# Kernel tuning notes

Hardware: AMD Instinct MI355X
Metric: run time of the kernel (lower is better)

The kernel has to match this reference:

```python
import jax, jax.numpy as jnp
import numpy as np

EMBED = 768
HEAD = 128

def setup_inputs() -> dict:
    key = jax.random.key(0)
    ks = jax.random.split(key, 8)
    B, S = 8, 2048
    x = jax.random.normal(ks[0], (B, S, EMBED), dtype=jnp.float32)
    enc_output = jax.random.normal(ks[1], (B, S, EMBED), dtype=jnp.float32)
    s = 1.0 / np.sqrt(EMBED)
    Wq = jax.random.normal(ks[2], (EMBED, HEAD), dtype=jnp.float32) * s
    Wk = jax.random.normal(ks[3], (EMBED, HEAD), dtype=jnp.float32) * s
    Wv = jax.random.normal(ks[4], (EMBED, HEAD), dtype=jnp.float32) * s
    bq = jnp.zeros((HEAD,), dtype=jnp.float32)
    bk = jnp.zeros((HEAD,), dtype=jnp.float32)
    bv = jnp.zeros((HEAD,), dtype=jnp.float32)
    return {"x": x, "enc_output": enc_output, "Wq": Wq, "bq": bq,
            "Wk": Wk, "bk": bk, "Wv": Wv, "bv": bv}

def reference(x, enc_output, Wq, bq, Wk, bk, Wv, bv):
    # Faithful to original: Q, K, V all from x (enc_output is unused in the
    # original forward); scale is embed_size ** 0.5; dropout never applied.
    q = jnp.einsum('nse,ed->nsd', x, Wq) + bq  # [B,S,H]
    k = jnp.einsum('nse,ed->nsd', x, Wk) + bk
    v = jnp.einsum('nse,ed->nsd', x, Wv) + bv
    energy = jnp.einsum('nqd,nkd->nqk', q, k)  # [B,S,S]
    attn = jax.nn.softmax(energy / jnp.sqrt(jnp.float32(EMBED)), axis=2)
    out = jnp.einsum('nql,nld->nqd', attn, v)  # [B,S,H]
    return out
```

## Files before the change

### kernel.cpp

```cpp
#include <hip/hip_runtime.h>
#include <hip/hip_bf16.h>


typedef __bf16 bf16x8 __attribute__((ext_vector_type(8)));
typedef float f32x4 __attribute__((ext_vector_type(4)));
using bf16 = __hip_bfloat16;

#define EMB 768
#define HD 128
#define SEQ 2048
#define BATCH 8
#define ROWS (BATCH * SEQ)
#define NSPLIT 4
#define TILES_PER_SPLIT (SEQ / 64 / NSPLIT)

__global__ __launch_bounds__(256) void wt_kernel(
    const float* __restrict__ Wq, const float* __restrict__ Wk,
    const float* __restrict__ Wv, bf16* __restrict__ Wt)
{
    __shared__ float t_lds[32][33];
    const int tid = threadIdx.x;
    const int k0 = blockIdx.x * 32;
    const int n0 = blockIdx.y * 32;
    const int mtx = blockIdx.z;
    const float* W = (mtx == 0) ? Wq : (mtx == 1) ? Wk : Wv;
    const int j = tid & 31, i0 = tid >> 5;
#pragma unroll
    for (int c = 0; c < 4; ++c)
        t_lds[i0 + 8 * c][j] = W[(size_t)(k0 + i0 + 8 * c) * HD + n0 + j];
    __syncthreads();
#pragma unroll
    for (int c = 0; c < 4; ++c)
        Wt[(size_t)mtx * HD * EMB + (size_t)(n0 + i0 + 8 * c) * EMB + k0 + j] =
            __float2bfloat16(t_lds[j][i0 + 8 * c]);
}

__global__ __launch_bounds__(256, 3) void qkv_kernel(
    const float* __restrict__ x, const bf16* __restrict__ Wt,
    const float* __restrict__ bq, const float* __restrict__ bk,
    const float* __restrict__ bv,
    bf16* __restrict__ Q, bf16* __restrict__ K, bf16* __restrict__ Vt)
{
    __shared__ alignas(16) bf16 b_lds[2][128 * 64];
    const int tid  = threadIdx.x;
    const int sel  = blockIdx.y;
    const int row0 = blockIdx.x * 64;
    const int lane = tid & 63, wave = tid >> 6;
    const int lr = lane & 15, lq = lane >> 4;

    const char* Wb = (const char*)(Wt + (size_t)sel * HD * EMB);
    const int rl = lane >> 3;
    const int chlog = (lane & 7) ^ rl;

    const float* arow = &x[(size_t)(row0 + wave * 16 + lr) * EMB + lq * 8];

    float4 araw[2][2];
    auto loadA = [&](int kt) {
#pragma unroll
        for (int ks = 0; ks < 2; ++ks) {
            const float* p = arow + kt * 64 + ks * 32;
            araw[ks][0] = *reinterpret_cast<const float4*>(p);
            araw[ks][1] = *reinterpret_cast<const float4*>(p + 4);
        }
    };
    auto stageB = [&](int kt, int pb) {
#pragma unroll
        for (int c = 0; c < 4; ++c) {
            int r = c * 32 + wave * 8 + rl;
            const char* src = Wb + (size_t)r * (EMB * 2) + kt * 128 + chlog * 16;
            bf16* dst = &b_lds[pb][(size_t)(c * 32 + wave * 8) * 64];
            __builtin_amdgcn_global_load_lds(
                (const __attribute__((address_space(1))) void*)src,
                (__attribute__((address_space(3))) void*)dst, 16, 0, 0);
        }
    };

    f32x4 acc[8];
#pragma unroll
    for (int j = 0; j < 8; ++j) acc[j] = f32x4{0.f, 0.f, 0.f, 0.f};

    stageB(0, 0);
    loadA(0);
    __syncthreads();

    for (int kt = 0; kt < EMB / 64; ++kt) {
        const int p = kt & 1;
        if (kt < 11) stageB(kt + 1, p ^ 1);
        bf16x8 af[2];
#pragma unroll
        for (int ks = 0; ks < 2; ++ks) {
            union { bf16 h[8]; bf16x8 v; } u;
            u.h[0] = __float2bfloat16(araw[ks][0].x);
            u.h[1] = __float2bfloat16(araw[ks][0].y);
            u.h[2] = __float2bfloat16(araw[ks][0].z);
            u.h[3] = __float2bfloat16(araw[ks][0].w);
            u.h[4] = __float2bfloat16(araw[ks][1].x);
            u.h[5] = __float2bfloat16(araw[ks][1].y);
            u.h[6] = __float2bfloat16(araw[ks][1].z);
            u.h[7] = __float2bfloat16(araw[ks][1].w);
            af[ks] = u.v;
        }
        if (kt < 11) loadA(kt + 1);
#pragma unroll
        for (int ks = 0; ks < 2; ++ks)
#pragma unroll
            for (int nt = 0; nt < 8; ++nt) {
                const bf16x8 b = *reinterpret_cast<const bf16x8*>(
                    &b_lds[p][((nt * 16 + lr) * 8 + ((ks * 4 + lq) ^ (lr & 7))) * 8]);
                acc[nt] = __builtin_amdgcn_mfma_f32_16x16x32_bf16(af[ks], b, acc[nt], 0, 0, 0);
            }
        __syncthreads();
    }

    bf16 (*o_lds)[132] = reinterpret_cast<bf16(*)[132]>(&b_lds[0][0]);
    const float* bias = (sel == 0) ? bq : (sel == 1) ? bk : bv;
#pragma unroll
    for (int nt = 0; nt < 8; ++nt) {
        int col = nt * 16 + lr;
        float bb = bias[col];
#pragma unroll
        for (int rg = 0; rg < 4; ++rg)
            o_lds[wave * 16 + lq * 4 + rg][col] = __float2bfloat16(acc[nt][rg] + bb);
    }
    __syncthreads();
    if (sel < 2) {
        bf16* dst = (sel == 0) ? Q : K;
#pragma unroll
        for (int c = 0; c < 4; ++c) {
            int lin = tid + c * 256;
            int r = lin >> 4, ch = lin & 15;
            *reinterpret_cast<uint4*>(&dst[(size_t)(row0 + r) * HD + ch * 8]) =
                *reinterpret_cast<const uint4*>(&o_lds[r][ch * 8]);
        }
    } else {
        int d = tid >> 1, sh = (tid & 1) * 32;
        int bi = row0 >> 11, s0 = row0 & (SEQ - 1);
        union { bf16 h[32]; uint4 u4[4]; } pk;
#pragma unroll
        for (int s = 0; s < 32; ++s) pk.h[s] = o_lds[sh + s][d];
        bf16* base = &Vt[((size_t)bi * HD + d) * SEQ + s0 + sh];
#pragma unroll
        for (int c = 0; c < 4; ++c)
            *reinterpret_cast<uint4*>(base + c * 8) = pk.u4[c];
    }
}

__global__ __launch_bounds__(256, 2) void flash_kernel(
    const bf16* __restrict__ Q, const bf16* __restrict__ K,
    const bf16* __restrict__ Vt,
    float* __restrict__ Opart, float* __restrict__ Lpart)
{
    __shared__ alignas(16) bf16 k_lds[64][132];
    __shared__ alignas(16) bf16 v_lds[144][68];
    __shared__ alignas(16) bf16 p_lds[4][32][72];
    const int tid = threadIdx.x;
    const int lane = tid & 63, wave = tid >> 6;
    const int lr = lane & 15, lq = lane >> 4;
    const int b  = blockIdx.y;
    const int split = blockIdx.z;
    const int q0 = blockIdx.x * 128;
    const int qrow = b * SEQ + q0 + wave * 32;

    const float sc = 0.03608439182435161f * 1.44269504088896f;

    for (int i = tid; i < 16 * 68; i += 256) {
        int r = i / 68, c = i % 68;
        v_lds[128 + r][c] = __float2bfloat16(r == 0 ? 1.0f : 0.0f);
    }

    bf16x8 qf[2][4];
#pragma unroll
    for (int qt = 0; qt < 2; ++qt)
#pragma unroll
        for (int ks = 0; ks < 4; ++ks)
            qf[qt][ks] = *reinterpret_cast<const bf16x8*>(
                &Q[(size_t)(qrow + qt * 16 + lr) * HD + ks * 32 + lq * 8]);

    f32x4 o[2][9];
#pragma unroll
    for (int qt = 0; qt < 2; ++qt)
#pragma unroll
        for (int d = 0; d < 9; ++d) o[qt][d] = f32x4{0.f, 0.f, 0.f, 0.f};

    for (int t = split * TILES_PER_SPLIT; t < (split + 1) * TILES_PER_SPLIT; ++t) {
        __syncthreads();
#pragma unroll
        for (int c = 0; c < 4; ++c) {
            int lin = tid + c * 256;
            int r = lin >> 4, ch = lin & 15;
            *reinterpret_cast<uint4*>(&k_lds[r][ch * 8]) =
                *reinterpret_cast<const uint4*>(&K[(size_t)(b * SEQ + t * 64 + r) * HD + ch * 8]);
        }
#pragma unroll
        for (int c = 0; c < 4; ++c) {
            int lin = tid + c * 256;
            int r = lin >> 3, ch = lin & 7;
            *reinterpret_cast<uint4*>(&v_lds[r][ch * 8]) =
                *reinterpret_cast<const uint4*>(&Vt[((size_t)b * HD + r) * SEQ + t * 64 + ch * 8]);
        }
        __syncthreads();

#pragma unroll
        for (int nt = 0; nt < 4; ++nt) {
            bf16x8 kf[4];
#pragma unroll
            for (int ks = 0; ks < 4; ++ks)
                kf[ks] = *reinterpret_cast<const bf16x8*>(&k_lds[nt * 16 + lr][ks * 32 + lq * 8]);
#pragma unroll
            for (int qt = 0; qt < 2; ++qt) {
                f32x4 s = f32x4{0.f, 0.f, 0.f, 0.f};
#pragma unroll
                for (int ks = 0; ks < 4; ++ks)
                    s = __builtin_amdgcn_mfma_f32_16x16x32_bf16(kf[ks], qf[qt][ks], s, 0, 0, 0);
                union { bf16 h[4]; uint2 u; } pk;
#pragma unroll
                for (int r = 0; r < 4; ++r)
                    pk.h[r] = __float2bfloat16(exp2f(__builtin_fmaf(s[r], sc, -8.0f)));
                *reinterpret_cast<uint2*>(&p_lds[wave][qt * 16 + lr][nt * 16 + lq * 4]) = pk.u;
            }
        }

#pragma unroll
        for (int ks = 0; ks < 2; ++ks) {
            bf16x8 pf[2];
#pragma unroll
            for (int qt = 0; qt < 2; ++qt)
                pf[qt] = *reinterpret_cast<const bf16x8*>(
                    &p_lds[wave][qt * 16 + lr][ks * 32 + lq * 8]);
#pragma unroll
            for (int d = 0; d < 9; ++d) {
                bf16x8 vf = *reinterpret_cast<const bf16x8*>(&v_lds[d * 16 + lr][ks * 32 + lq * 8]);
#pragma unroll
                for (int qt = 0; qt < 2; ++qt)
                    o[qt][d] = __builtin_amdgcn_mfma_f32_16x16x32_bf16(vf, pf[qt], o[qt][d], 0, 0, 0);
            }
        }
    }

    const size_t obase = (size_t)split * ROWS;
#pragma unroll
    for (int qt = 0; qt < 2; ++qt) {
#pragma unroll
        for (int d = 0; d < 8; ++d)
            *reinterpret_cast<f32x4*>(
                &Opart[(obase + qrow + qt * 16 + lr) * HD + d * 16 + lq * 4]) = o[qt][d];
        if (lane < 16)
            Lpart[obase + qrow + qt * 16 + lr] = o[qt][8][0];
    }
}

__global__ __launch_bounds__(256) void combine_kernel(
    const float* __restrict__ Opart, const float* __restrict__ Lpart,
    float* __restrict__ out)
{
    int gid = blockIdx.x * 256 + threadIdx.x;
    int row = gid >> 5, dc = gid & 31;
    float L = 0.f;
#pragma unroll
    for (int s = 0; s < NSPLIT; ++s)
        L += Lpart[(size_t)s * ROWS + row];
    float4 acc = {0.f, 0.f, 0.f, 0.f};
#pragma unroll
    for (int s = 0; s < NSPLIT; ++s) {
        float4 v = *reinterpret_cast<const float4*>(&Opart[((size_t)s * ROWS + row) * HD + dc * 4]);
        acc.x += v.x; acc.y += v.y; acc.z += v.z; acc.w += v.w;
    }
    float inv = 1.f / L;
    acc.x *= inv; acc.y *= inv; acc.z *= inv; acc.w *= inv;
    *reinterpret_cast<float4*>(&out[(size_t)row * HD + dc * 4]) = acc;
}

extern "C" void kernel_launch(void* const* d_in, const int* in_sizes, int n_in,
                              void* d_out, int out_size, void* d_ws, size_t ws_size,
                              hipStream_t stream) {
    const float* x  = (const float*)d_in[0];
    const float* Wq = (const float*)d_in[2];
    const float* bq = (const float*)d_in[3];
    const float* Wk = (const float*)d_in[4];
    const float* bk = (const float*)d_in[5];
    const float* Wv = (const float*)d_in[6];
    const float* bv = (const float*)d_in[7];
    float* out = (float*)d_out;

    char* ws = (char*)d_ws;
    const size_t WT_BYTES  = (size_t)3 * HD * EMB * 2;
    const size_t QKV_BYTES = (size_t)ROWS * HD * 2;
    const size_t OP_BYTES  = (size_t)NSPLIT * ROWS * HD * 4;
    bf16*  Wt    = (bf16*)ws;
    bf16*  Qb    = (bf16*)(ws + WT_BYTES);
    bf16*  Kb    = (bf16*)(ws + WT_BYTES + QKV_BYTES);
    bf16*  Vt    = (bf16*)(ws + WT_BYTES + 2 * QKV_BYTES);
    float* Opart = (float*)(ws + WT_BYTES + 3 * QKV_BYTES);
    float* Lpart = (float*)(ws + WT_BYTES + 3 * QKV_BYTES + OP_BYTES);

    hipLaunchKernelGGL(wt_kernel, dim3(EMB / 32, HD / 32, 3), dim3(256), 0, stream,
                       Wq, Wk, Wv, Wt);
    hipLaunchKernelGGL(qkv_kernel, dim3(ROWS / 64, 3), dim3(256), 0, stream,
                       x, Wt, bq, bk, bv, Qb, Kb, Vt);
    hipLaunchKernelGGL(flash_kernel, dim3(SEQ / 128, BATCH, NSPLIT), dim3(256), 0, stream,
                       Qb, Kb, Vt, Opart, Lpart);
    hipLaunchKernelGGL(combine_kernel, dim3(ROWS * 32 / 256), dim3(256), 0, stream,
                       Opart, Lpart, out);
}
```

Measured before the change: 181.8 us.

## Fuse Q, K, V projections into one block per row tile

The QKV projection kernel now computes all three outputs in one 512-thread block: 8 waves split as 4 row groups by 2 column halves of the 384-wide concatenated weight. Each x row tile is read and converted to bf16 once instead of three times, and the grid drops its third dimension. The cost is doubled LDS per block for the B tiles (96KB double buffer), 12 accumulators per wave, and a reworked epilogue that writes Q, K and the transposed V from one staging buffer. Lower occupancy could limit the gain.

Measured after the change: 183.8 us. Within noise of the previous version (+1.1%).

```diff
diff --git a/kernel.cpp b/kernel.cpp
--- a/kernel.cpp
+++ b/kernel.cpp
@@ -35,24 +35,25 @@
             __float2bfloat16(t_lds[j][i0 + 8 * c]);
 }
 
-__global__ __launch_bounds__(256, 3) void qkv_kernel(
+__global__ __launch_bounds__(512, 2) void qkv_kernel(
     const float* __restrict__ x, const bf16* __restrict__ Wt,
     const float* __restrict__ bq, const float* __restrict__ bk,
     const float* __restrict__ bv,
     bf16* __restrict__ Q, bf16* __restrict__ K, bf16* __restrict__ Vt)
 {
-    __shared__ alignas(16) bf16 b_lds[2][128 * 64];
+    __shared__ alignas(16) bf16 b_lds[2][384 * 64];
     const int tid  = threadIdx.x;
-    const int sel  = blockIdx.y;
     const int row0 = blockIdx.x * 64;
     const int lane = tid & 63, wave = tid >> 6;
     const int lr = lane & 15, lq = lane >> 4;
-
-    const char* Wb = (const char*)(Wt + (size_t)sel * HD * EMB);
+    const int wr = wave >> 1;
+    const int cw = wave & 1;
+
+    const char* Wb = (const char*)Wt;
     const int rl = lane >> 3;
     const int chlog = (lane & 7) ^ rl;
 
-    const float* arow = &x[(size_t)(row0 + wave * 16 + lr) * EMB + lq * 8];
+    const float* arow = &x[(size_t)(row0 + wr * 16 + lr) * EMB + lq * 8];
 
     float4 araw[2][2];
     auto loadA = [&](int kt) {
@@ -65,19 +66,19 @@
     };
     auto stageB = [&](int kt, int pb) {
 #pragma unroll
-        for (int c = 0; c < 4; ++c) {
-            int r = c * 32 + wave * 8 + rl;
+        for (int c = 0; c < 6; ++c) {
+            int r = c * 64 + wave * 8 + rl;
             const char* src = Wb + (size_t)r * (EMB * 2) + kt * 128 + chlog * 16;
-            bf16* dst = &b_lds[pb][(size_t)(c * 32 + wave * 8) * 64];
+            bf16* dst = &b_lds[pb][(size_t)(c * 64 + wave * 8) * 64];
             __builtin_amdgcn_global_load_lds(
                 (const __attribute__((address_space(1))) void*)src,
                 (__attribute__((address_space(3))) void*)dst, 16, 0, 0);
         }
     };
 
-    f32x4 acc[8];
-#pragma unroll
-    for (int j = 0; j < 8; ++j) acc[j] = f32x4{0.f, 0.f, 0.f, 0.f};
+    f32x4 acc[12];
+#pragma unroll
+    for (int j = 0; j < 12; ++j) acc[j] = f32x4{0.f, 0.f, 0.f, 0.f};
 
     stageB(0, 0);
     loadA(0);
@@ -104,44 +105,47 @@
 #pragma unroll
         for (int ks = 0; ks < 2; ++ks)
 #pragma unroll
-            for (int nt = 0; nt < 8; ++nt) {
+            for (int nt = 0; nt < 12; ++nt) {
                 const bf16x8 b = *reinterpret_cast<const bf16x8*>(
-                    &b_lds[p][((nt * 16 + lr) * 8 + ((ks * 4 + lq) ^ (lr & 7))) * 8]);
+                    &b_lds[p][((cw * 192 + nt * 16 + lr) * 8 + ((ks * 4 + lq) ^ (lr & 7))) * 8]);
                 acc[nt] = __builtin_amdgcn_mfma_f32_16x16x32_bf16(af[ks], b, acc[nt], 0, 0, 0);
             }
         __syncthreads();
     }
 
-    bf16 (*o_lds)[132] = reinterpret_cast<bf16(*)[132]>(&b_lds[0][0]);
-    const float* bias = (sel == 0) ? bq : (sel == 1) ? bk : bv;
-#pragma unroll
-    for (int nt = 0; nt < 8; ++nt) {
-        int col = nt * 16 + lr;
-        float bb = bias[col];
-#pragma unroll
-        for (int rg = 0; rg < 4; ++rg)
-            o_lds[wave * 16 + lq * 4 + rg][col] = __float2bfloat16(acc[nt][rg] + bb);
+    bf16* o_lds = &b_lds[0][0];
+    {
+#pragma unroll
+        for (int nt = 0; nt < 12; ++nt) {
+            int colb = cw * 192 + nt * 16;
+            int m = colb >> 7;
+            const float* bp = (m == 0) ? bq : (m == 1) ? bk : bv;
+            float bb = bp[(colb & 127) + lr];
+#pragma unroll
+            for (int rg = 0; rg < 4; ++rg)
+                o_lds[(wr * 16 + lq * 4 + rg) * 400 + colb + lr] =
+                    __float2bfloat16(acc[nt][rg] + bb);
+        }
     }
     __syncthreads();
-    if (sel < 2) {
-        bf16* dst = (sel == 0) ? Q : K;
-#pragma unroll
-        for (int c = 0; c < 4; ++c) {
-            int lin = tid + c * 256;
-            int r = lin >> 4, ch = lin & 15;
-            *reinterpret_cast<uint4*>(&dst[(size_t)(row0 + r) * HD + ch * 8]) =
-                *reinterpret_cast<const uint4*>(&o_lds[r][ch * 8]);
-        }
-    } else {
-        int d = tid >> 1, sh = (tid & 1) * 32;
+#pragma unroll
+    for (int c = 0; c < 4; ++c) {
+        int lin = c * 512 + tid;
+        int r = lin >> 5, ch = lin & 31;
+        uint4 v = *reinterpret_cast<const uint4*>(&o_lds[r * 400 + ch * 8]);
+        bf16* dst = (ch < 16) ? &Q[(size_t)(row0 + r) * HD + ch * 8]
+                              : &K[(size_t)(row0 + r) * HD + (ch - 16) * 8];
+        *reinterpret_cast<uint4*>(dst) = v;
+    }
+    {
+        int d = tid >> 2, sh = (tid & 3) * 16;
         int bi = row0 >> 11, s0 = row0 & (SEQ - 1);
-        union { bf16 h[32]; uint4 u4[4]; } pk;
-#pragma unroll
-        for (int s = 0; s < 32; ++s) pk.h[s] = o_lds[sh + s][d];
+        union { bf16 h[16]; uint4 u4[2]; } pk;
+#pragma unroll
+        for (int i = 0; i < 16; ++i) pk.h[i] = o_lds[(sh + i) * 400 + 256 + d];
         bf16* base = &Vt[((size_t)bi * HD + d) * SEQ + s0 + sh];
-#pragma unroll
-        for (int c = 0; c < 4; ++c)
-            *reinterpret_cast<uint4*>(base + c * 8) = pk.u4[c];
+        *reinterpret_cast<uint4*>(base)     = pk.u4[0];
+        *reinterpret_cast<uint4*>(base + 8) = pk.u4[1];
     }
 }
 
@@ -295,7 +299,7 @@
 
     hipLaunchKernelGGL(wt_kernel, dim3(EMB / 32, HD / 32, 3), dim3(256), 0, stream,
                        Wq, Wk, Wv, Wt);
-    hipLaunchKernelGGL(qkv_kernel, dim3(ROWS / 64, 3), dim3(256), 0, stream,
+    hipLaunchKernelGGL(qkv_kernel, dim3(ROWS / 64), dim3(512), 0, stream,
                        x, Wt, bq, bk, bv, Qb, Kb, Vt);
     hipLaunchKernelGGL(flash_kernel, dim3(SEQ / 128, BATCH, NSPLIT), dim3(256), 0, stream,
                        Qb, Kb, Vt, Opart, Lpart);
```

## Double-buffer K/V tiles with direct global-to-LDS loads and 512-thread blocks

Applied to the files above, without the earlier changes.

The flash kernel now stages K and V tiles into two LDS buffers with the direct global-to-LDS load builtin, prefetching the next tile while the current one is computed, and drops one of the two barriers per iteration. LDS rows use an XOR swizzle instead of padding to avoid bank conflicts. Blocks grow to 512 threads covering 256 query rows, so each K/V tile is shared by twice as many waves. The cost is higher LDS use per block, which may limit occupancy, and reliance on the async-load ordering being correct without an explicit wait.

Measured after the change: 182.6 us. About the same (+0.4%).

```diff
diff --git a/kernel.cpp b/kernel.cpp
--- a/kernel.cpp
+++ b/kernel.cpp
@@ -145,28 +145,56 @@
     }
 }
 
-__global__ __launch_bounds__(256, 2) void flash_kernel(
+__global__ __launch_bounds__(512, 2) void flash_kernel(
     const bf16* __restrict__ Q, const bf16* __restrict__ K,
     const bf16* __restrict__ Vt,
     float* __restrict__ Opart, float* __restrict__ Lpart)
 {
-    __shared__ alignas(16) bf16 k_lds[64][132];
-    __shared__ alignas(16) bf16 v_lds[144][68];
-    __shared__ alignas(16) bf16 p_lds[4][32][72];
+    __shared__ alignas(16) bf16 k_lds[2][64][128];
+    __shared__ alignas(16) bf16 v_lds[2][144][64];
+    __shared__ alignas(16) bf16 p_lds[8][32][72];
     const int tid = threadIdx.x;
     const int lane = tid & 63, wave = tid >> 6;
     const int lr = lane & 15, lq = lane >> 4;
     const int b  = blockIdx.y;
     const int split = blockIdx.z;
-    const int q0 = blockIdx.x * 128;
+    const int q0 = blockIdx.x * 256;
     const int qrow = b * SEQ + q0 + wave * 32;
 
     const float sc = 0.03608439182435161f * 1.44269504088896f;
 
-    for (int i = tid; i < 16 * 68; i += 256) {
-        int r = i / 68, c = i % 68;
-        v_lds[128 + r][c] = __float2bfloat16(r == 0 ? 1.0f : 0.0f);
-    }
+    for (int i = tid; i < 2 * 16 * 64; i += 512) {
+        int pb = i >> 10, r = (i >> 6) & 15, c = i & 63;
+        v_lds[pb][128 + r][c] = __float2bfloat16(r == 0 ? 1.0f : 0.0f);
+    }
+
+    const int rl16 = lane >> 4, sl16 = lane & 15;
+    const int rl8  = lane >> 3, sl8  = lane & 7;
+
+    auto stage = [&](int t, int pb) {
+#pragma unroll
+        for (int c = 0; c < 2; ++c) {
+            int rbase = c * 32 + wave * 4;
+            int r = rbase + rl16;
+            int ch = sl16 ^ (r & 7);
+            const bf16* src = &K[(size_t)(b * SEQ + t * 64 + r) * HD + ch * 8];
+            bf16* dst = &k_lds[pb][rbase][0];
+            __builtin_amdgcn_global_load_lds(
+                (const __attribute__((address_space(1))) void*)src,
+                (__attribute__((address_space(3))) void*)dst, 16, 0, 0);
+        }
+#pragma unroll
+        for (int c = 0; c < 2; ++c) {
+            int rbase = c * 64 + wave * 8;
+            int r = rbase + rl8;
+            int ch = sl8 ^ (r & 7);
+            const bf16* src = &Vt[((size_t)b * HD + r) * SEQ + t * 64 + ch * 8];
+            bf16* dst = &v_lds[pb][rbase][0];
+            __builtin_amdgcn_global_load_lds(
+                (const __attribute__((address_space(1))) void*)src,
+                (__attribute__((address_space(3))) void*)dst, 16, 0, 0);
+        }
+    };
 
     bf16x8 qf[2][4];
 #pragma unroll
@@ -182,30 +210,21 @@
 #pragma unroll
         for (int d = 0; d < 9; ++d) o[qt][d] = f32x4{0.f, 0.f, 0.f, 0.f};
 
-    for (int t = split * TILES_PER_SPLIT; t < (split + 1) * TILES_PER_SPLIT; ++t) {
-        __syncthreads();
-#pragma unroll
-        for (int c = 0; c < 4; ++c) {
-            int lin = tid + c * 256;
-            int r = lin >> 4, ch = lin & 15;
-            *reinterpret_cast<uint4*>(&k_lds[r][ch * 8]) =
-                *reinterpret_cast<const uint4*>(&K[(size_t)(b * SEQ + t * 64 + r) * HD + ch * 8]);
-        }
-#pragma unroll
-        for (int c = 0; c < 4; ++c) {
-            int lin = tid + c * 256;
-            int r = lin >> 3, ch = lin & 7;
-            *reinterpret_cast<uint4*>(&v_lds[r][ch * 8]) =
-                *reinterpret_cast<const uint4*>(&Vt[((size_t)b * HD + r) * SEQ + t * 64 + ch * 8]);
-        }
-        __syncthreads();
+    const int t0 = split * TILES_PER_SPLIT, t1 = t0 + TILES_PER_SPLIT;
+    stage(t0, 0);
+    __syncthreads();
+
+    for (int t = t0; t < t1; ++t) {
+        const int pb = (t - t0) & 1;
+        if (t + 1 < t1) stage(t + 1, pb ^ 1);
 
 #pragma unroll
         for (int nt = 0; nt < 4; ++nt) {
             bf16x8 kf[4];
 #pragma unroll
             for (int ks = 0; ks < 4; ++ks)
-                kf[ks] = *reinterpret_cast<const bf16x8*>(&k_lds[nt * 16 + lr][ks * 32 + lq * 8]);
+                kf[ks] = *reinterpret_cast<const bf16x8*>(
+                    &k_lds[pb][nt * 16 + lr][((ks * 4 + lq) ^ (lr & 7)) * 8]);
 #pragma unroll
             for (int qt = 0; qt < 2; ++qt) {
                 f32x4 s = f32x4{0.f, 0.f, 0.f, 0.f};
@@ -229,12 +248,14 @@
                     &p_lds[wave][qt * 16 + lr][ks * 32 + lq * 8]);
 #pragma unroll
             for (int d = 0; d < 9; ++d) {
-                bf16x8 vf = *reinterpret_cast<const bf16x8*>(&v_lds[d * 16 + lr][ks * 32 + lq * 8]);
+                bf16x8 vf = *reinterpret_cast<const bf16x8*>(
+                    &v_lds[pb][d * 16 + lr][((ks * 4 + lq) ^ (lr & 7)) * 8]);
 #pragma unroll
                 for (int qt = 0; qt < 2; ++qt)
                     o[qt][d] = __builtin_amdgcn_mfma_f32_16x16x32_bf16(vf, pf[qt], o[qt][d], 0, 0, 0);
             }
         }
+        __syncthreads();
     }
 
     const size_t obase = (size_t)split * ROWS;
@@ -297,7 +318,7 @@
                        Wq, Wk, Wv, Wt);
     hipLaunchKernelGGL(qkv_kernel, dim3(ROWS / 64, 3), dim3(256), 0, stream,
                        x, Wt, bq, bk, bv, Qb, Kb, Vt);
-    hipLaunchKernelGGL(flash_kernel, dim3(SEQ / 128, BATCH, NSPLIT), dim3(256), 0, stream,
+    hipLaunchKernelGGL(flash_kernel, dim3(SEQ / 256, BATCH, NSPLIT), dim3(512), 0, stream,
                        Qb, Kb, Vt, Opart, Lpart);
     hipLaunchKernelGGL(combine_kernel, dim3(ROWS * 32 / 256), dim3(256), 0, stream,
                        Opart, Lpart, out);
```
